# Performance work log

Measured on AMD Instinct MI355X. Metric: run time of the kernel, lower is better.

The kernel has to match this reference:

```python
import jax, jax.numpy as jnp
import numpy as np

N_CODES = 65536  # 2**(n_bits*codebook_dim) = 2**(2*8)
CB_DIM = 8


def setup_inputs() -> dict:
    key = jax.random.key(0)
    k1, k2 = jax.random.split(key)
    x = jax.random.normal(k1, (16, 2048), dtype=jnp.float32)
    codebook = jax.random.normal(k2, (N_CODES, CB_DIM), dtype=jnp.float32)
    return {"x": x, "codebook": codebook}


def reference(x, codebook):
    # per-row scaling factor (detached in torch; forward value identical)
    scale = jnp.mean(jnp.abs(x), axis=1, keepdims=True)  # [B, 1]
    u = x / scale
    flat = u.reshape(-1, codebook.shape[1])  # [M, d]

    # squared euclidean distances (argmin is identical to cdist argmin)
    d2 = (
        jnp.sum(flat * flat, axis=1, keepdims=True)
        - 2.0 * flat @ codebook.T
        + jnp.sum(codebook * codebook, axis=1)
    )  # [M, N]
    indices = jnp.argmin(d2, axis=1)  # [M]

    # EMA-style codebook replacement: cluster means with count clamp
    sums = jax.ops.segment_sum(flat, indices, num_segments=codebook.shape[0])
    counts = jax.ops.segment_sum(
        jnp.ones((flat.shape[0],), dtype=jnp.float32), indices,
        num_segments=codebook.shape[0])
    new_codebook = sums / jnp.clip(counts, 1.0, None)[:, None]

    quantized = new_codebook[indices].reshape(x.shape)
    return scale * quantized
```

## Files before the change

kernel.cpp:

```cpp
#include <hip/hip_runtime.h>
#include <stdint.h>

#define N_CODES 65536
#define CB_DIM 8
#define B_ROWS 16
#define X_COLS 2048
#define M_ROWS 4096
#define RPB 8
#define THREADS 256

#define WS_SCALE 0
#define WS_IDX   256
#define WS_U     16640
#define WS_SUMS  147712
#define WS_CNT   2244864

#define CODE_BODY(C0, C1, NIDX)                                            \
    {                                                                      \
        float hn = (C0).x * (C0).x;                                        \
        hn = fmaf((C0).y, (C0).y, hn);                                     \
        hn = fmaf((C0).z, (C0).z, hn);                                     \
        hn = fmaf((C0).w, (C0).w, hn);                                     \
        hn = fmaf((C1).x, (C1).x, hn);                                     \
        hn = fmaf((C1).y, (C1).y, hn);                                     \
        hn = fmaf((C1).z, (C1).z, hn);                                     \
        hn = fmaf((C1).w, (C1).w, hn);                                     \
        _Pragma("unroll")                                                  \
        for (int r = 0; r < RPB; r++) {                                    \
            float d = hn;                                                  \
            d = fmaf(nu[r * 8 + 0], (C0).x, d);                            \
            d = fmaf(nu[r * 8 + 1], (C0).y, d);                            \
            d = fmaf(nu[r * 8 + 2], (C0).z, d);                            \
            d = fmaf(nu[r * 8 + 3], (C0).w, d);                            \
            d = fmaf(nu[r * 8 + 4], (C1).x, d);                            \
            d = fmaf(nu[r * 8 + 5], (C1).y, d);                            \
            d = fmaf(nu[r * 8 + 6], (C1).z, d);                            \
            d = fmaf(nu[r * 8 + 7], (C1).w, d);                            \
            if (d < best[r]) { best[r] = d; bidx[r] = (NIDX); }            \
        }                                                                  \
    }

__global__ __launch_bounds__(256, 2) void argmin_kernel(const float* __restrict__ x,
                                                        const float* __restrict__ cb,
                                                        float* __restrict__ scale_out,
                                                        int* __restrict__ indices,
                                                        float* __restrict__ uout,
                                                        float* __restrict__ sums,
                                                        float* __restrict__ counts) {
    int tid = threadIdx.x;
    int m0 = blockIdx.x * RPB;
    int xr = m0 >> 8;

    const float4* xv = (const float4*)(x + xr * X_COLS);
    float4 q0 = xv[tid];
    float4 q1 = xv[tid + 256];
    float s = fabsf(q0.x) + fabsf(q0.y) + fabsf(q0.z) + fabsf(q0.w)
            + fabsf(q1.x) + fabsf(q1.y) + fabsf(q1.z) + fabsf(q1.w);
    #pragma unroll
    for (int off = 32; off > 0; off >>= 1) s += __shfl_down(s, off, 64);
    __shared__ float ls[4];
    __shared__ float scale_sh;
    int wave = tid >> 6, lane = tid & 63;
    if (lane == 0) ls[wave] = s;
    __syncthreads();
    if (tid == 0) {
        float t = (ls[0] + ls[1] + ls[2] + ls[3]) * (1.0f / (float)X_COLS);
        scale_sh = t;
        if ((blockIdx.x & 31) == 0) scale_out[xr] = t;
    }
    __syncthreads();
    float scale = scale_sh;

    __shared__ float u_sh[RPB * CB_DIM];
    if (tid < RPB * CB_DIM) {
        int col = (m0 & 255) * CB_DIM + tid;
        float u = x[xr * X_COLS + col] / scale;
        u_sh[tid] = u;
        uout[m0 * CB_DIM + tid] = u;
    }
    __syncthreads();

    float nu[RPB * CB_DIM];
    #pragma unroll
    for (int i = 0; i < RPB * CB_DIM; i++) {
        float v = -2.0f * u_sh[i];
        nu[i] = __uint_as_float(__builtin_amdgcn_readfirstlane(__float_as_uint(v)));
    }

    float best[RPB];
    int   bidx[RPB];
    #pragma unroll
    for (int r = 0; r < RPB; r++) { best[r] = 3.4e38f; bidx[r] = 0; }

    const float4* cp = (const float4*)cb;
    float4 a0 = cp[2 * tid],             a1 = cp[2 * tid + 1];
    float4 b0 = cp[2 * (tid + THREADS)], b1 = cp[2 * (tid + THREADS) + 1];

    int n = tid;
    for (int k = 0; k < 127; k++, n += 2 * THREADS) {
        float4 pa0 = cp[2 * (n + 2 * THREADS)], pa1 = cp[2 * (n + 2 * THREADS) + 1];
        CODE_BODY(a0, a1, n)
        float4 pb0 = cp[2 * (n + 3 * THREADS)], pb1 = cp[2 * (n + 3 * THREADS) + 1];
        CODE_BODY(b0, b1, n + THREADS)
        a0 = pa0; a1 = pa1; b0 = pb0; b1 = pb1;
    }
    CODE_BODY(a0, a1, n)
    CODE_BODY(b0, b1, n + THREADS)

    __shared__ unsigned long long red[RPB][THREADS];
    #pragma unroll
    for (int r = 0; r < RPB; r++) {
        unsigned int b = __float_as_uint(best[r]);
        unsigned int k = b ^ ((unsigned int)((int)b >> 31) | 0x80000000u);
        red[r][tid] = ((unsigned long long)k << 32) | (unsigned int)bidx[r];
    }
    for (int t = THREADS / 2; t > 0; t >>= 1) {
        __syncthreads();
        if (tid < t) {
            #pragma unroll
            for (int r = 0; r < RPB; r++) {
                unsigned long long a = red[r][tid], c = red[r][tid + t];
                if (c < a) red[r][tid] = c;
            }
        }
    }
    __syncthreads();

    if (tid < RPB) {
        int idx = (int)(red[tid][0] & 0xFFFFFFFFull);
        indices[m0 + tid] = idx;
        counts[idx] = 0.f;
        float4 z = make_float4(0.f, 0.f, 0.f, 0.f);
        float4* sp = (float4*)(sums + (size_t)idx * CB_DIM);
        sp[0] = z;
        sp[1] = z;
    }
}

__global__ __launch_bounds__(256) void accum_kernel(const int* __restrict__ indices,
                                                    const float* __restrict__ u,
                                                    float* __restrict__ sums,
                                                    float* __restrict__ counts) {
    int e = blockIdx.x * blockDim.x + threadIdx.x;
    int m = e >> 3, k = e & 7;
    int idx = indices[m];
    if (k == 0) atomicAdd(&counts[idx], 1.0f);
    atomicAdd(&sums[(size_t)idx * CB_DIM + k], u[e]);
}

__global__ __launch_bounds__(256) void gather_kernel(const int* __restrict__ indices,
                                                     const float* __restrict__ sums,
                                                     const float* __restrict__ counts,
                                                     const float* __restrict__ scale,
                                                     float* __restrict__ out) {
    int e = blockIdx.x * blockDim.x + threadIdx.x;
    if (e < B_ROWS * X_COLS) {
        int m = e >> 3, k = e & 7;
        int idx = indices[m];
        float c = counts[idx];
        c = c < 1.f ? 1.f : c;
        out[e] = scale[e >> 11] * (sums[(size_t)idx * CB_DIM + k] / c);
    }
}

extern "C" void kernel_launch(void* const* d_in, const int* in_sizes, int n_in,
                              void* d_out, int out_size, void* d_ws, size_t ws_size,
                              hipStream_t stream) {
    const float* x  = (const float*)d_in[0];
    const float* cb = (const float*)d_in[1];
    char* ws = (char*)d_ws;
    float* scale   = (float*)(ws + WS_SCALE);
    int*   indices = (int*)(ws + WS_IDX);
    float* u       = (float*)(ws + WS_U);
    float* sums    = (float*)(ws + WS_SUMS);
    float* counts  = (float*)(ws + WS_CNT);
    float* out     = (float*)d_out;

    argmin_kernel<<<M_ROWS / RPB, 256, 0, stream>>>(x, cb, scale, indices, u, sums, counts);
    accum_kernel <<<(M_ROWS * CB_DIM) / 256, 256, 0, stream>>>(indices, u, sums, counts);
    gather_kernel<<<(B_ROWS * X_COLS) / 256, 256, 0, stream>>>(indices, sums, counts, scale, out);
}
```

Before: 136.8 us.

## Split scaling into prep kernel and deepen codebook prefetch to four codes

Moves the per-row abs-mean scale and the -2*u vector into a separate prep kernel, so each argmin block no longer redoes the 2048-element row reduction and its two block barriers. The argmin loop now keeps four code pairs in flight instead of two, for deeper load latency hiding at the cost of more registers. Accumulation now sums -2*u, and the gather multiplies by -0.5 to undo it. This adds a kernel launch, and the nu values are now read from global memory per lane instead of via readfirstlane, which may cost scalar-register uniformity.

```diff
diff --git a/kernel.cpp b/kernel.cpp
--- a/kernel.cpp
+++ b/kernel.cpp
@@ -40,17 +40,11 @@
         }                                                                  \
     }
 
-__global__ __launch_bounds__(256, 2) void argmin_kernel(const float* __restrict__ x,
-                                                        const float* __restrict__ cb,
-                                                        float* __restrict__ scale_out,
-                                                        int* __restrict__ indices,
-                                                        float* __restrict__ uout,
-                                                        float* __restrict__ sums,
-                                                        float* __restrict__ counts) {
+__global__ __launch_bounds__(256) void prep_kernel(const float* __restrict__ x,
+                                                   float* __restrict__ scale_out,
+                                                   float* __restrict__ nuout) {
     int tid = threadIdx.x;
-    int m0 = blockIdx.x * RPB;
-    int xr = m0 >> 8;
-
+    int xr = blockIdx.x;
     const float4* xv = (const float4*)(x + xr * X_COLS);
     float4 q0 = xv[tid];
     float4 q1 = xv[tid + 256];
@@ -66,26 +60,33 @@
     if (tid == 0) {
         float t = (ls[0] + ls[1] + ls[2] + ls[3]) * (1.0f / (float)X_COLS);
         scale_sh = t;
-        if ((blockIdx.x & 31) == 0) scale_out[xr] = t;
+        scale_out[xr] = t;
     }
     __syncthreads();
     float scale = scale_sh;
 
-    __shared__ float u_sh[RPB * CB_DIM];
-    if (tid < RPB * CB_DIM) {
-        int col = (m0 & 255) * CB_DIM + tid;
-        float u = x[xr * X_COLS + col] / scale;
-        u_sh[tid] = u;
-        uout[m0 * CB_DIM + tid] = u;
-    }
-    __syncthreads();
+    float4 n0, n1;
+    n0.x = -2.0f * (q0.x / scale);  n0.y = -2.0f * (q0.y / scale);
+    n0.z = -2.0f * (q0.z / scale);  n0.w = -2.0f * (q0.w / scale);
+    n1.x = -2.0f * (q1.x / scale);  n1.y = -2.0f * (q1.y / scale);
+    n1.z = -2.0f * (q1.z / scale);  n1.w = -2.0f * (q1.w / scale);
+    float4* np = (float4*)(nuout + xr * X_COLS);
+    np[tid]       = n0;
+    np[tid + 256] = n1;
+}
 
+__global__ __launch_bounds__(256, 2) void argmin_kernel(const float* __restrict__ cb,
+                                                        const float* __restrict__ nuarr,
+                                                        int* __restrict__ indices,
+                                                        float* __restrict__ sums,
+                                                        float* __restrict__ counts) {
+    int tid = threadIdx.x;
+    int m0 = blockIdx.x * RPB;
+
+    const float* __restrict__ up = nuarr + (size_t)m0 * CB_DIM;
     float nu[RPB * CB_DIM];
     #pragma unroll
-    for (int i = 0; i < RPB * CB_DIM; i++) {
-        float v = -2.0f * u_sh[i];
-        nu[i] = __uint_as_float(__builtin_amdgcn_readfirstlane(__float_as_uint(v)));
-    }
+    for (int i = 0; i < RPB * CB_DIM; i++) nu[i] = up[i];
 
     float best[RPB];
     int   bidx[RPB];
@@ -93,19 +94,27 @@
     for (int r = 0; r < RPB; r++) { best[r] = 3.4e38f; bidx[r] = 0; }
 
     const float4* cp = (const float4*)cb;
-    float4 a0 = cp[2 * tid],             a1 = cp[2 * tid + 1];
-    float4 b0 = cp[2 * (tid + THREADS)], b1 = cp[2 * (tid + THREADS) + 1];
+    int n = tid;
+    float4 a0 = cp[2 * n],           a1 = cp[2 * n + 1];
+    float4 b0 = cp[2 * (n + 256)],   b1 = cp[2 * (n + 256) + 1];
+    float4 c0 = cp[2 * (n + 512)],   c1 = cp[2 * (n + 512) + 1];
+    float4 d0 = cp[2 * (n + 768)],   d1 = cp[2 * (n + 768) + 1];
 
-    int n = tid;
-    for (int k = 0; k < 127; k++, n += 2 * THREADS) {
-        float4 pa0 = cp[2 * (n + 2 * THREADS)], pa1 = cp[2 * (n + 2 * THREADS) + 1];
+    for (int j = 0; j < 63; j++) {
         CODE_BODY(a0, a1, n)
-        float4 pb0 = cp[2 * (n + 3 * THREADS)], pb1 = cp[2 * (n + 3 * THREADS) + 1];
-        CODE_BODY(b0, b1, n + THREADS)
-        a0 = pa0; a1 = pa1; b0 = pb0; b1 = pb1;
+        CODE_BODY(b0, b1, n + 256)
+        a0 = cp[2 * (n + 1024)]; a1 = cp[2 * (n + 1024) + 1];
+        b0 = cp[2 * (n + 1280)]; b1 = cp[2 * (n + 1280) + 1];
+        CODE_BODY(c0, c1, n + 512)
+        CODE_BODY(d0, d1, n + 768)
+        c0 = cp[2 * (n + 1536)]; c1 = cp[2 * (n + 1536) + 1];
+        d0 = cp[2 * (n + 1792)]; d1 = cp[2 * (n + 1792) + 1];
+        n += 1024;
     }
     CODE_BODY(a0, a1, n)
-    CODE_BODY(b0, b1, n + THREADS)
+    CODE_BODY(b0, b1, n + 256)
+    CODE_BODY(c0, c1, n + 512)
+    CODE_BODY(d0, d1, n + 768)
 
     __shared__ unsigned long long red[RPB][THREADS];
     #pragma unroll
@@ -138,14 +147,14 @@
 }
 
 __global__ __launch_bounds__(256) void accum_kernel(const int* __restrict__ indices,
-                                                    const float* __restrict__ u,
+                                                    const float* __restrict__ nuarr,
                                                     float* __restrict__ sums,
                                                     float* __restrict__ counts) {
     int e = blockIdx.x * blockDim.x + threadIdx.x;
     int m = e >> 3, k = e & 7;
     int idx = indices[m];
     if (k == 0) atomicAdd(&counts[idx], 1.0f);
-    atomicAdd(&sums[(size_t)idx * CB_DIM + k], u[e]);
+    atomicAdd(&sums[(size_t)idx * CB_DIM + k], nuarr[e]);
 }
 
 __global__ __launch_bounds__(256) void gather_kernel(const int* __restrict__ indices,
@@ -159,7 +168,7 @@
         int idx = indices[m];
         float c = counts[idx];
         c = c < 1.f ? 1.f : c;
-        out[e] = scale[e >> 11] * (sums[(size_t)idx * CB_DIM + k] / c);
+        out[e] = scale[e >> 11] * (-0.5f * (sums[(size_t)idx * CB_DIM + k] / c));
     }
 }
 
@@ -171,12 +180,13 @@
     char* ws = (char*)d_ws;
     float* scale   = (float*)(ws + WS_SCALE);
     int*   indices = (int*)(ws + WS_IDX);
-    float* u       = (float*)(ws + WS_U);
+    float* nuarr   = (float*)(ws + WS_U);
     float* sums    = (float*)(ws + WS_SUMS);
     float* counts  = (float*)(ws + WS_CNT);
     float* out     = (float*)d_out;
 
-    argmin_kernel<<<M_ROWS / RPB, 256, 0, stream>>>(x, cb, scale, indices, u, sums, counts);
-    accum_kernel <<<(M_ROWS * CB_DIM) / 256, 256, 0, stream>>>(indices, u, sums, counts);
+    prep_kernel  <<<B_ROWS, 256, 0, stream>>>(x, scale, nuarr);
+    argmin_kernel<<<M_ROWS / RPB, 256, 0, stream>>>(cb, nuarr, indices, sums, counts);
+    accum_kernel <<<(M_ROWS * CB_DIM) / 256, 256, 0, stream>>>(indices, nuarr, sums, counts);
     gather_kernel<<<(B_ROWS * X_COLS) / 256, 256, 0, stream>>>(indices, sums, counts, scale, out);
 }
```

Result: slower. 164.9 us (+20.5%).
